# Kernel optimization log

Measured on AMD Instinct MI355X. Metric: run time of the kernel, lower is better.

## Reference

```python
import jax, jax.numpy as jnp
import numpy as np

B, L, E, MODES = 32, 1024, 512, 64


def setup_inputs() -> dict:
    key = jax.random.key(0)
    k1, k2, k3 = jax.random.split(key, 3)
    scale = 1.0 / (E * E)
    q = jax.random.normal(k1, (B, L, E), dtype=jnp.float32)
    # torch.rand(..., dtype=cfloat) -> real and imag each uniform [0,1)
    w_real = scale * jax.random.uniform(k2, (E, E, MODES), dtype=jnp.float32)
    w_imag = scale * jax.random.uniform(k3, (E, E, MODES), dtype=jnp.float32)
    return {"q": q, "w_real": w_real, "w_imag": w_imag}


def reference(q, w_real, w_imag):
    # mode_select_method='lowest': index = [0..MODES-1], sorted
    index = jnp.arange(MODES)
    x = jnp.transpose(q, (0, 2, 1))            # [B, E, L]
    x_ft = jnp.fft.rfft(x, axis=-1)            # [B, E, L//2+1] complex
    xg = x_ft[:, :, index]                     # gather selected modes [B, E, M]
    W = w_real + 1j * w_imag                   # [E_in, E_out, M] complex
    # fused batched complex GEMM over all modes (replaces per-mode loop)
    out_modes = jnp.einsum('bhm,him->bim', xg, W)  # [B, E, M]
    F = L // 2 + 1
    out_ft = jnp.zeros((B, E, F), dtype=out_modes.dtype)
    # original writes results at positions wi = 0..M-1 (loop index), not at `index`
    out_ft = out_ft.at[:, :, :MODES].set(out_modes)
    x_out = jnp.fft.irfft(out_ft, n=L, axis=-1)    # [B, E, L] real
    return jnp.transpose(x_out, (0, 2, 1))         # [B, L, E]
```

## Files before the change

### kernel.cpp

```cpp
#include <hip/hip_runtime.h>
#include <math.h>

#define LQ 1024
#define EQ 512
#define BQ 32
#define MQ 64

static constexpr int BCHUNK = LQ * EQ;

typedef short short8 __attribute__((ext_vector_type(8)));
typedef float f32x4 __attribute__((ext_vector_type(4)));
typedef unsigned short ushort_t;

union FragI { int i[4]; int4 v; short8 s; };

__device__ inline char* sx_ptr(float* dout, int arr, int m, int b, int h) {
    unsigned G = ((unsigned)arr << 20) + ((unsigned)m << 14) +
                 ((unsigned)(h >> 5) << 10) + ((unsigned)b << 5) + (unsigned)(h & 31);
    unsigned z = G >> 19, w = G & 524287u;
    return (char*)(dout + (size_t)z * BCHUNK + 262144) + (size_t)w * 2;
}

__device__ inline void split2(float a, float b, unsigned& hi, unsigned& lo) {
    unsigned ua = __float_as_uint(a), ub = __float_as_uint(b);
    unsigned ha = ua & 0xFFFF0000u, hb = ub & 0xFFFF0000u;
    hi = (ua >> 16) | hb;
    float la = a - __uint_as_float(ha);
    float lb = b - __uint_as_float(hb);
    lo = (__float_as_uint(la) >> 16) | (__float_as_uint(lb) & 0xFFFF0000u);
}

__device__ inline void split1(float x, ushort_t& hi, ushort_t& lo) {
    unsigned u = __float_as_uint(x);
    hi = (ushort_t)(u >> 16);
    float r = x - __uint_as_float(u & 0xFFFF0000u);
    lo = (ushort_t)(__float_as_uint(r) >> 16);
}

__global__ __launch_bounds__(256) void k_trig(unsigned* __restrict__ BFhi,
                                              unsigned* __restrict__ BFlo,
                                              float* __restrict__ dout) {
    int idx = blockIdx.x * 256 + threadIdx.x;
    int l = idx >> 6, m = idx & 63;
    int tt = (l * m) & (LQ - 1);
    float ang = (float)tt * 6.135923151542565e-03f;
    float s, c;
    sincosf(ang, &s, &c);
    float coef = (m == 0 ? 1.0f : 2.0f) * (1.0f / (float)LQ);
    float b0 = coef * c;
    float b1 = (m == 0) ? 0.0f : (-2.0f / (float)LQ) * s;
    unsigned hi, lo;
    split2(b0, b1, hi, lo);
    {
        int lt = l >> 4, kb = m >> 4, kgb = (m & 15) >> 2;
        int lane = kgb * 16 + (l & 15);
        int u = lt * 1024 + kb * 256 + lane * 4 + (m & 3);
        BFhi[u] = hi;
        BFlo[u] = lo;
    }
    ushort_t* THs = (ushort_t*)dout;
    ushort_t* TLs = (ushort_t*)(dout + 65536);
    int ks = l >> 5, kg = (l >> 3) & 3, j = l & 7;
    int mt = m >> 3;
    int lane0 = kg * 16 + 2 * (m & 7);
    ushort_t ch, cl, sh, sl;
    split1(c, ch, cl);
    split1(-s, sh, sl);
    int u0 = ((ks * 8 + mt) * 64 + lane0) * 8 + j;
    THs[u0] = ch;  TLs[u0] = cl;
    THs[u0 + 8] = sh;  TLs[u0 + 8] = sl;
}

__global__ __launch_bounds__(512) void k_dft3(const float* __restrict__ q,
                                              float* __restrict__ dout) {
    __shared__ float qs[64][34];
    const int t    = threadIdx.x;
    const int wave = t >> 6;
    const int lane = t & 63;
    const int a    = wave & 3;
    const int ht   = wave >> 2;
    const int b    = blockIdx.x >> 4;
    const int hg   = blockIdx.x & 15;
    const int hbase = hg * 32;
    const int col  = lane & 15;
    const int kg   = lane >> 4;
    const float* qb = q + (size_t)b * BCHUNK;
    const int4* TH4 = (const int4*)dout;
    const int4* TL4 = (const int4*)(dout + 65536);

    f32x4 acc[2] = {{0.f, 0.f, 0.f, 0.f}, {0.f, 0.f, 0.f, 0.f}};
    float2 st2[2];
#define LOADQ(CC)                                                             \
    {                                                                         \
        int l0_ = (CC) * 64;                                                  \
        _Pragma("unroll")                                                     \
        for (int r = 0; r < 2; ++r) {                                         \
            int e = r * 512 + t;                                              \
            int lp = e >> 4, hc = (e & 15) * 2;                               \
            st2[r] = *(const float2*)&qb[(size_t)(l0_ + lp) * EQ + hbase + hc]; \
        }                                                                     \
    }

    LOADQ(0);
#define MM(A, B, C) C = __builtin_amdgcn_mfma_f32_16x16x32_bf16(A, B, C, 0, 0, 0)
    for (int cchunk = 0; cchunk < 16; ++cchunk) {
#pragma unroll
        for (int r = 0; r < 2; ++r) {
            int e = r * 512 + t;
            int lp = e >> 4, hc = (e & 15) * 2;
            *(float2*)&qs[lp][hc] = st2[r];
        }
        __syncthreads();
        if (cchunk < 15) LOADQ(cchunk + 1);
#pragma unroll
        for (int ksl = 0; ksl < 2; ++ksl) {
            const int ks = cchunk * 2 + ksl;
            float v[8];
#pragma unroll
            for (int j = 0; j < 8; ++j)
                v[j] = qs[ksl * 32 + kg * 8 + j][ht * 16 + col];
            FragI bhiF, bloF;
#pragma unroll
            for (int k = 0; k < 4; ++k) {
                unsigned h_, l_;
                split2(v[2 * k], v[2 * k + 1], h_, l_);
                bhiF.i[k] = (int)h_;
                bloF.i[k] = (int)l_;
            }
#pragma unroll
            for (int ti = 0; ti < 2; ++ti) {
                int mt = 2 * a + ti;
                FragI ah, al;
                ah.v = TH4[(ks * 8 + mt) * 64 + lane];
                al.v = TL4[(ks * 8 + mt) * 64 + lane];
                MM(ah.s, bhiF.s, acc[ti]);
                MM(ah.s, bloF.s, acc[ti]);
                MM(al.s, bhiF.s, acc[ti]);
            }
        }
        __syncthreads();
    }
#undef MM
#undef LOADQ
    const int h = hbase + ht * 16 + col;
#pragma unroll
    for (int ti = 0; ti < 2; ++ti) {
        int mt = 2 * a + ti;
        int mA = mt * 8 + kg * 2;
#pragma unroll
        for (int mi = 0; mi < 2; ++mi) {
            float xr = acc[ti][2 * mi];
            float xi = acc[ti][2 * mi + 1];
            ushort_t rh, rl, ih_, il_;
            split1(xr, rh, rl);
            split1(xi, ih_, il_);
            int m = mA + mi;
            *(ushort_t*)sx_ptr(dout, 0, m, b, h) = rh;
            *(ushort_t*)sx_ptr(dout, 1, m, b, h) = rl;
            *(ushort_t*)sx_ptr(dout, 2, m, b, h) = ih_;
            *(ushort_t*)sx_ptr(dout, 3, m, b, h) = il_;
        }
    }
}

__global__ __launch_bounds__(512) void k_modes6(const float* __restrict__ wreal,
                                                const float* __restrict__ wimag,
                                                float* __restrict__ dout) {
    __shared__ float Wlds[2 * 32 * 16 * 18];
    const int t    = threadIdx.x;
    const int wave = t >> 6;
    const int lane = t & 63;
    const int p    = blockIdx.x;
    const int blk  = (p & 7) * 64 + (p >> 3);
    const int hs   = blk >> 7;
    const int mc   = (blk >> 5) & 3;
    const int it   = blk & 31;
    const int i0   = it * 16;
    const int m0   = mc * 16;
    const int col  = lane & 15;
    const int kg   = lane >> 4;
    const int hbase = hs * 128;

    const char* xp0 = sx_ptr(dout, 0, m0 + 2 * wave, col, hbase + kg * 8);

    f32x4 zero4 = {0.f, 0.f, 0.f, 0.f};
    f32x4 acc[2][2][2];
#pragma unroll
    for (int a = 0; a < 2; ++a)
#pragma unroll
        for (int bq = 0; bq < 2; ++bq)
#pragma unroll
            for (int c = 0; c < 2; ++c) acc[a][bq][c] = zero4;

    float2 st[16];
#define LOADK(KK)                                                             \
    {                                                                         \
        int h0_ = hbase + (KK) * 32;                                          \
        _Pragma("unroll")                                                     \
        for (int r = 0; r < 16; ++r) {                                        \
            int e = r * 512 + t;                                              \
            int m2 = e & 7, ii = (e >> 3) & 15, hh = (e >> 7) & 31;           \
            const float* src = (e >> 12) ? wimag : wreal;                     \
            st[r] = *(const float2*)&src[(size_t)(h0_ + hh) * 32768 +         \
                                         (size_t)(i0 + ii) * 64 + m0 + 2 * m2]; \
        }                                                                     \
    }

    LOADK(0);
    for (int kk = 0; kk < 4; ++kk) {
#pragma unroll
        for (int r = 0; r < 16; ++r) {
            int e = r * 512 + t;
            int m2 = e & 7, ii = (e >> 3) & 15, hh = (e >> 7) & 31;
            int part = e >> 12;
            *(float2*)&Wlds[(((part * 32 + hh) * 16) + ii) * 18 + 2 * m2] = st[r];
        }
        __syncthreads();
        if (kk < 3) LOADK(kk + 1);
#pragma unroll
        for (int mi = 0; mi < 2; ++mi) {
            const int mloc = 2 * wave + mi;
            short8 aW[2][2];
            short8 nW[2];
#pragma unroll
            for (int part = 0; part < 2; ++part) {
                float v[8];
#pragma unroll
                for (int j = 0; j < 8; ++j)
                    v[j] = Wlds[((part * 32 + kg * 8 + j) * 16 + col) * 18 + mloc];
                FragI hiF, loF;
#pragma unroll
                for (int k = 0; k < 4; ++k) {
                    unsigned h, l;
                    split2(v[2 * k], v[2 * k + 1], h, l);
                    hiF.i[k] = (int)h;
                    loF.i[k] = (int)l;
                }
                aW[part][0] = hiF.s;
                aW[part][1] = loF.s;
                if (part == 1) {
                    FragI nh, nl;
#pragma unroll
                    for (int k = 0; k < 4; ++k) {
                        nh.i[k] = hiF.i[k] ^ 0x80008000;
                        nl.i[k] = loF.i[k] ^ 0x80008000;
                    }
                    nW[0] = nh.s;
                    nW[1] = nl.s;
                }
            }
            const char* xpm = xp0 + (size_t)mi * 32768 + (size_t)kk * 2048;
#define MM(A, B, C) C = __builtin_amdgcn_mfma_f32_16x16x32_bf16(A, B, C, 0, 0, 0)
#pragma unroll
            for (int nt = 0; nt < 2; ++nt) {
                short8 bX[4];
#pragma unroll
                for (int arr = 0; arr < 4; ++arr) {
                    FragI f;
                    f.v = *(const int4*)(xpm + (size_t)arr * 4194304 +
                                         (size_t)nt * 1024);
                    bX[arr] = f.s;
                }
                MM(aW[0][0], bX[0], acc[mi][0][nt]);
                MM(aW[0][0], bX[1], acc[mi][0][nt]);
                MM(aW[0][1], bX[0], acc[mi][0][nt]);
                MM(nW[0],    bX[2], acc[mi][0][nt]);
                MM(nW[0],    bX[3], acc[mi][0][nt]);
                MM(nW[1],    bX[2], acc[mi][0][nt]);
                MM(aW[0][0], bX[2], acc[mi][1][nt]);
                MM(aW[0][0], bX[3], acc[mi][1][nt]);
                MM(aW[0][1], bX[2], acc[mi][1][nt]);
                MM(aW[1][0], bX[0], acc[mi][1][nt]);
                MM(aW[1][0], bX[1], acc[mi][1][nt]);
                MM(aW[1][1], bX[0], acc[mi][1][nt]);
            }
#undef MM
        }
        __syncthreads();
    }
#undef LOADK
#pragma unroll
    for (int mi = 0; mi < 2; ++mi)
#pragma unroll
        for (int part = 0; part < 2; ++part)
#pragma unroll
            for (int nt = 0; nt < 2; ++nt) {
                int bb = nt * 16 + col;
                int c = 2 * (m0 + 2 * wave + mi) + part;
                f32x4 vv = acc[mi][part][nt];
                float4 o = make_float4(vv.x, vv.y, vv.z, vv.w);
                *(float4*)&dout[(size_t)bb * BCHUNK + (size_t)hs * 65536 +
                                (size_t)c * EQ + i0 + kg * 4] = o;
            }
}

__global__ __launch_bounds__(256) void k_inv3(const unsigned* __restrict__ BFhi,
                                              const unsigned* __restrict__ BFlo,
                                              float* __restrict__ dout) {
    __shared__ unsigned Bf[4096];
    const int t    = threadIdx.x;
    const int wave = t >> 6;
    const int lane = t & 63;
    const int b    = blockIdx.x >> 4;
    const int it   = blockIdx.x & 15;
    const int i0   = it * 32;
    float* base = dout + (size_t)b * BCHUNK;

#pragma unroll
    for (int r = 0; r < 8; ++r) {
        int idx = r * 256 + t;
        int il = idx & 31, cp = idx >> 5;
        int c0 = 2 * cp;
        const float* p0 = base + (size_t)c0 * EQ + i0 + il;
        float s0 = p0[0] + p0[65536] + p0[2 * 65536] + p0[3 * 65536];
        const float* p1 = p0 + EQ;
        float s1 = p1[0] + p1[65536] + p1[2 * 65536] + p1[3 * 65536];
        unsigned hi, lo;
        split2(s0, s1, hi, lo);
        int nt = il >> 4, i_loc = il & 15;
        int kb = c0 >> 5, kg = (c0 & 31) >> 3, jp = (c0 & 7) >> 1;
        int u = (nt * 4 + kb) * 256 + (kg * 16 + i_loc) * 4 + jp;
        Bf[u] = hi;
        Bf[2048 + u] = lo;
    }
    __syncthreads();
    FragI bh[2][4], bl[2][4];
#pragma unroll
    for (int nt = 0; nt < 2; ++nt)
#pragma unroll
        for (int kb = 0; kb < 4; ++kb) {
            bh[nt][kb].v = *(const int4*)&Bf[(nt * 4 + kb) * 256 + lane * 4];
            bl[nt][kb].v = *(const int4*)&Bf[2048 + (nt * 4 + kb) * 256 + lane * 4];
        }
#define MM(A, B, C) C = __builtin_amdgcn_mfma_f32_16x16x32_bf16(A, B, C, 0, 0, 0)
    for (int r = 0; r < 16; ++r) {
        int lt = wave + 4 * r;
        FragI ah[4], al[4];
#pragma unroll
        for (int kb = 0; kb < 4; ++kb) {
            ah[kb].v = *(const int4*)&BFhi[lt * 1024 + kb * 256 + lane * 4];
            al[kb].v = *(const int4*)&BFlo[lt * 1024 + kb * 256 + lane * 4];
        }
        f32x4 a0 = {0.f, 0.f, 0.f, 0.f}, a1 = {0.f, 0.f, 0.f, 0.f};
#pragma unroll
        for (int kb = 0; kb < 4; ++kb) {
            MM(ah[kb].s, bh[0][kb].s, a0);
            MM(ah[kb].s, bl[0][kb].s, a0);
            MM(al[kb].s, bh[0][kb].s, a0);
            MM(ah[kb].s, bh[1][kb].s, a1);
            MM(ah[kb].s, bl[1][kb].s, a1);
            MM(al[kb].s, bh[1][kb].s, a1);
        }
        int lrow = lt * 16 + (lane >> 4) * 4;
        int icol = i0 + (lane & 15);
#pragma unroll
        for (int j = 0; j < 4; ++j) {
            base[(size_t)(lrow + j) * EQ + icol]      = a0[j];
            base[(size_t)(lrow + j) * EQ + icol + 16] = a1[j];
        }
    }
#undef MM
}

extern "C" void kernel_launch(void* const* d_in, const int* in_sizes, int n_in,
                              void* d_out, int out_size, void* d_ws, size_t ws_size,
                              hipStream_t stream) {
    const float* q  = (const float*)d_in[0];
    const float* wr = (const float*)d_in[1];
    const float* wi = (const float*)d_in[2];
    float* out = (float*)d_out;
    unsigned* BFhi = (unsigned*)d_ws;
    unsigned* BFlo = BFhi + 65536;

    hipLaunchKernelGGL(k_trig,   dim3(256), dim3(256), 0, stream, BFhi, BFlo, out);
    hipLaunchKernelGGL(k_dft3,   dim3(512), dim3(512), 0, stream, q, out);
    hipLaunchKernelGGL(k_modes6, dim3(512), dim3(512), 0, stream, wr, wi, out);
    hipLaunchKernelGGL(k_inv3,   dim3(512), dim3(256), 0, stream, BFhi, BFlo, out);
}
```

Measured before the change: 148.8 us.

## Double-buffer DFT input via direct global-to-LDS loads and prefetch twiddles

The forward DFT kernel now stages q tiles into a double-buffered LDS array using global_load_lds, which skips the register round-trip, and drops one barrier per chunk. Twiddle fragments for both k-slices are loaded at the top of each iteration, before the MFMAs that use them. The modes kernel also drops its block-index swizzle and uses blockIdx directly. The risks are the unpadded LDS layout causing bank conflicts, a possible race because only one barrier remains per iteration, and worse L2 locality without the swizzle.

```diff
diff --git a/kernel.cpp b/kernel.cpp
--- a/kernel.cpp
+++ b/kernel.cpp
@@ -13,6 +13,12 @@
 typedef unsigned short ushort_t;
 
 union FragI { int i[4]; int4 v; short8 s; };
+
+__device__ __forceinline__ void gload16(const float* g, float* l) {
+    __builtin_amdgcn_global_load_lds(
+        (const __attribute__((address_space(1))) void*)g,
+        (__attribute__((address_space(3))) void*)l, 16, 0, 0);
+}
 
 __device__ inline char* sx_ptr(float* dout, int arr, int m, int b, int h) {
     unsigned G = ((unsigned)arr << 20) + ((unsigned)m << 14) +
@@ -71,9 +77,11 @@
     THs[u0 + 8] = sh;  TLs[u0 + 8] = sl;
 }
 
-__global__ __launch_bounds__(512) void k_dft3(const float* __restrict__ q,
+#define MM(A, B, C) C = __builtin_amdgcn_mfma_f32_16x16x32_bf16(A, B, C, 0, 0, 0)
+
+__global__ __launch_bounds__(512) void k_dft4(const float* __restrict__ q,
                                               float* __restrict__ dout) {
-    __shared__ float qs[64][34];
+    __shared__ float qs[2 * 2048];
     const int t    = threadIdx.x;
     const int wave = t >> 6;
     const int lane = t & 63;
@@ -89,59 +97,49 @@
     const int4* TL4 = (const int4*)(dout + 65536);
 
     f32x4 acc[2] = {{0.f, 0.f, 0.f, 0.f}, {0.f, 0.f, 0.f, 0.f}};
-    float2 st2[2];
-#define LOADQ(CC)                                                             \
-    {                                                                         \
-        int l0_ = (CC) * 64;                                                  \
-        _Pragma("unroll")                                                     \
-        for (int r = 0; r < 2; ++r) {                                         \
-            int e = r * 512 + t;                                              \
-            int lp = e >> 4, hc = (e & 15) * 2;                               \
-            st2[r] = *(const float2*)&qb[(size_t)(l0_ + lp) * EQ + hbase + hc]; \
-        }                                                                     \
-    }
-
-    LOADQ(0);
-#define MM(A, B, C) C = __builtin_amdgcn_mfma_f32_16x16x32_bf16(A, B, C, 0, 0, 0)
-    for (int cchunk = 0; cchunk < 16; ++cchunk) {
-#pragma unroll
-        for (int r = 0; r < 2; ++r) {
-            int e = r * 512 + t;
-            int lp = e >> 4, hc = (e & 15) * 2;
-            *(float2*)&qs[lp][hc] = st2[r];
-        }
+    const int lp = wave * 8 + (lane >> 3);
+    const int hq = 4 * (lane & 7);
+
+    gload16(qb + (size_t)lp * EQ + hbase + hq, &qs[wave * 256]);
+
+    int cur = 0;
+    for (int cc = 0; cc < 16; ++cc) {
         __syncthreads();
-        if (cchunk < 15) LOADQ(cchunk + 1);
+        FragI ah[2][2], al[2][2];
+#pragma unroll
+        for (int ksl = 0; ksl < 2; ++ksl)
+#pragma unroll
+            for (int ti = 0; ti < 2; ++ti) {
+                int idx = ((cc * 2 + ksl) * 8 + 2 * a + ti) * 64 + lane;
+                ah[ksl][ti].v = TH4[idx];
+                al[ksl][ti].v = TL4[idx];
+            }
+        if (cc < 15)
+            gload16(qb + (size_t)((cc + 1) * 64 + lp) * EQ + hbase + hq,
+                    &qs[(cur ^ 1) * 2048 + wave * 256]);
 #pragma unroll
         for (int ksl = 0; ksl < 2; ++ksl) {
-            const int ks = cchunk * 2 + ksl;
             float v[8];
 #pragma unroll
             for (int j = 0; j < 8; ++j)
-                v[j] = qs[ksl * 32 + kg * 8 + j][ht * 16 + col];
+                v[j] = qs[cur * 2048 + (ksl * 32 + kg * 8 + j) * 32 + ht * 16 + col];
             FragI bhiF, bloF;
 #pragma unroll
-            for (int k = 0; k < 4; ++k) {
+            for (int k2 = 0; k2 < 4; ++k2) {
                 unsigned h_, l_;
-                split2(v[2 * k], v[2 * k + 1], h_, l_);
-                bhiF.i[k] = (int)h_;
-                bloF.i[k] = (int)l_;
+                split2(v[2 * k2], v[2 * k2 + 1], h_, l_);
+                bhiF.i[k2] = (int)h_;
+                bloF.i[k2] = (int)l_;
             }
 #pragma unroll
             for (int ti = 0; ti < 2; ++ti) {
-                int mt = 2 * a + ti;
-                FragI ah, al;
-                ah.v = TH4[(ks * 8 + mt) * 64 + lane];
-                al.v = TL4[(ks * 8 + mt) * 64 + lane];
-                MM(ah.s, bhiF.s, acc[ti]);
-                MM(ah.s, bloF.s, acc[ti]);
-                MM(al.s, bhiF.s, acc[ti]);
-            }
-        }
-        __syncthreads();
-    }
-#undef MM
-#undef LOADQ
+                MM(ah[ksl][ti].s, bhiF.s, acc[ti]);
+                MM(ah[ksl][ti].s, bloF.s, acc[ti]);
+                MM(al[ksl][ti].s, bhiF.s, acc[ti]);
+            }
+        }
+        cur ^= 1;
+    }
     const int h = hbase + ht * 16 + col;
 #pragma unroll
     for (int ti = 0; ti < 2; ++ti) {
@@ -163,15 +161,14 @@
     }
 }
 
-__global__ __launch_bounds__(512) void k_modes6(const float* __restrict__ wreal,
-                                                const float* __restrict__ wimag,
-                                                float* __restrict__ dout) {
+__global__ __launch_bounds__(512) void k_modes11(const float* __restrict__ wreal,
+                                                 const float* __restrict__ wimag,
+                                                 float* __restrict__ dout) {
     __shared__ float Wlds[2 * 32 * 16 * 18];
     const int t    = threadIdx.x;
     const int wave = t >> 6;
     const int lane = t & 63;
-    const int p    = blockIdx.x;
-    const int blk  = (p & 7) * 64 + (p >> 3);
+    const int blk  = blockIdx.x;
     const int hs   = blk >> 7;
     const int mc   = (blk >> 5) & 3;
     const int it   = blk & 31;
@@ -250,7 +247,6 @@
                 }
             }
             const char* xpm = xp0 + (size_t)mi * 32768 + (size_t)kk * 2048;
-#define MM(A, B, C) C = __builtin_amdgcn_mfma_f32_16x16x32_bf16(A, B, C, 0, 0, 0)
 #pragma unroll
             for (int nt = 0; nt < 2; ++nt) {
                 short8 bX[4];
@@ -274,7 +270,6 @@
                 MM(aW[1][0], bX[1], acc[mi][1][nt]);
                 MM(aW[1][1], bX[0], acc[mi][1][nt]);
             }
-#undef MM
         }
         __syncthreads();
     }
@@ -332,7 +327,6 @@
             bh[nt][kb].v = *(const int4*)&Bf[(nt * 4 + kb) * 256 + lane * 4];
             bl[nt][kb].v = *(const int4*)&Bf[2048 + (nt * 4 + kb) * 256 + lane * 4];
         }
-#define MM(A, B, C) C = __builtin_amdgcn_mfma_f32_16x16x32_bf16(A, B, C, 0, 0, 0)
     for (int r = 0; r < 16; ++r) {
         int lt = wave + 4 * r;
         FragI ah[4], al[4];
@@ -359,8 +353,8 @@
             base[(size_t)(lrow + j) * EQ + icol + 16] = a1[j];
         }
     }
+}
 #undef MM
-}
 
 extern "C" void kernel_launch(void* const* d_in, const int* in_sizes, int n_in,
                               void* d_out, int out_size, void* d_ws, size_t ws_size,
@@ -372,8 +366,8 @@
     unsigned* BFhi = (unsigned*)d_ws;
     unsigned* BFlo = BFhi + 65536;
 
-    hipLaunchKernelGGL(k_trig,   dim3(256), dim3(256), 0, stream, BFhi, BFlo, out);
-    hipLaunchKernelGGL(k_dft3,   dim3(512), dim3(512), 0, stream, q, out);
-    hipLaunchKernelGGL(k_modes6, dim3(512), dim3(512), 0, stream, wr, wi, out);
-    hipLaunchKernelGGL(k_inv3,   dim3(512), dim3(256), 0, stream, BFhi, BFlo, out);
-}
+    hipLaunchKernelGGL(k_trig,    dim3(256), dim3(256), 0, stream, BFhi, BFlo, out);
+    hipLaunchKernelGGL(k_dft4,    dim3(512), dim3(512), 0, stream, q, out);
+    hipLaunchKernelGGL(k_modes11, dim3(512), dim3(512), 0, stream, wr, wi, out);
+    hipLaunchKernelGGL(k_inv3,    dim3(512), dim3(256), 0, stream, BFhi, BFlo, out);
+}
```

Result: faster. 127.8 us (-14.1%).
